# Kernel optimization log

Measured on AMD Instinct MI355X. Metric: run time of the kernel, lower is better.

The kernel has to match this reference:

```python
import jax, jax.numpy as jnp
import numpy as np
from jax import lax

# dims: B=2, C=dim=64, H=W=128 -> N=16384 tokens; d_inner=128, d_state=16, dt_rank=4, d_conv=4

def setup_inputs() -> dict:
    key = jax.random.key(0)
    ks = jax.random.split(key, 8)
    def n(k, shp, scale=0.02):
        return jax.random.normal(k, shp, jnp.float32) * scale
    d_inner, d_state, dt_rank = 128, 16, 4
    return {
        "x": jax.random.normal(ks[0], (2, 64, 128, 128), jnp.float32),
        "ln_w": jnp.ones((64,), jnp.float32),
        "ln_b": jnp.zeros((64,), jnp.float32),
        "in_proj_w": n(ks[1], (2 * d_inner, 64)),
        "conv_w": n(ks[2], (d_inner, 1, 4), 0.1),
        "conv_b": jnp.zeros((d_inner,), jnp.float32),
        "x_proj_w": n(ks[3], (dt_rank + 2 * d_state, d_inner)),
        "dt_proj_w": n(ks[4], (d_inner, dt_rank), 0.5),
        "dt_proj_b": n(ks[5], (d_inner,), 0.1),
        "A_log": jnp.log(jnp.broadcast_to(jnp.arange(1, d_state + 1, dtype=jnp.float32), (d_inner, d_state))),
        "D_param": jnp.ones((d_inner,), jnp.float32),
        "out_proj_w": n(ks[6], (64, d_inner)),
        "out_proj_b": jnp.zeros((64,), jnp.float32),
    }


def reference(x, ln_w, ln_b, in_proj_w, conv_w, conv_b, x_proj_w,
              dt_proj_w, dt_proj_b, A_log, D_param, out_proj_w, out_proj_b):
    B, C, H, W = x.shape
    d_inner = in_proj_w.shape[0] // 2
    d_state = A_log.shape[1]
    dt_rank = dt_proj_w.shape[1]
    eps = 1e-5

    # feature2token + channel LayerNorm (Restormer WithBias LN over C)
    t = x.reshape(B, C, H * W).transpose(0, 2, 1)  # [B, N, C]
    mu = jnp.mean(t, axis=-1, keepdims=True)
    var = jnp.var(t, axis=-1, keepdims=True)
    t = (t - mu) * lax.rsqrt(var + eps) * ln_w + ln_b

    # in_proj -> x, z
    xz = jnp.einsum('bnc,dc->bnd', t, in_proj_w)  # [B, N, 2*d_inner]
    x_in, z = jnp.split(xz, 2, axis=-1)

    # depthwise causal conv1d (k=4, pad left 3), then SiLU
    u = lax.conv_general_dilated(
        x_in.transpose(0, 2, 1), conv_w,
        window_strides=(1,), padding=[(3, 0)],
        feature_group_count=d_inner,
        dimension_numbers=('NCH', 'OIH', 'NCH'))
    u = jax.nn.silu(u + conv_b[None, :, None]).transpose(0, 2, 1)  # [B, N, d_inner]

    # x_proj -> dt, B, C of the SSM
    x_dbl = jnp.einsum('bnd,ed->bne', u, x_proj_w)
    dt_r = x_dbl[..., :dt_rank]
    Bmat = x_dbl[..., dt_rank:dt_rank + d_state]   # [B, N, d_state]
    Cmat = x_dbl[..., dt_rank + d_state:]          # [B, N, d_state]
    dt = jax.nn.softplus(jnp.einsum('bnr,dr->bnd', dt_r, dt_proj_w) + dt_proj_b)

    # selective scan: h_t = exp(dt*A) h_{t-1} + dt*B*u
    A = -jnp.exp(A_log)  # [d_inner, d_state]
    deltaA = jnp.exp(jnp.einsum('bnd,ds->bnds', dt, A))
    deltaBu = jnp.einsum('bnd,bns,bnd->bnds', dt, Bmat, u)

    def combine(c1, c2):
        a1, b1 = c1
        a2, b2 = c2
        return a2 * a1, a2 * b1 + b2

    _, h = lax.associative_scan(combine, (deltaA, deltaBu), axis=1)  # h: [B, N, d_inner, d_state]

    y = jnp.einsum('bnds,bns->bnd', h, Cmat) + u * D_param
    y = y * jax.nn.silu(z)
    out = jnp.einsum('bnd,cd->bnc', y, out_proj_w) + out_proj_b  # [B, N, C]

    # token2feature
    return out.transpose(0, 2, 1).reshape(B, C, H, W)
```

## Files before the change

kernel.cpp:

```cpp
#include <hip/hip_runtime.h>
#include <math.h>

#define NTOK 16384
#define DIN  128
#define NCH  512
#define CHL  32
#define NG   32
#define GCH  16

__device__ __forceinline__ float silu_f(float x)    { return x / (1.f + __expf(-x)); }
__device__ __forceinline__ float softplus_f(float x){ return (x > 20.f) ? x : log1pf(__expf(x)); }

__global__ __launch_bounds__(256) void k1_ln_inproj(
    const float* __restrict__ x, const float* __restrict__ lnw,
    const float* __restrict__ lnb, const float* __restrict__ Win,
    float* __restrict__ xin, float* __restrict__ zbuf)
{
  __shared__ __align__(16) float bufW[128*68];
  __shared__ __align__(16) float bufB[64*68];
  __shared__ float ps[256], pq[256], mu[64], rs[64];

  int t = threadIdx.x;
  int b  = blockIdx.x >> 8;
  int n0 = (blockIdx.x & 255) << 6;
  const float* xb = x + ((size_t)b*64)*NTOK;

  int tok = t & 63, quad = t >> 6;
  float s0 = 0.f, s1 = 0.f;
  for (int i = 0; i < 16; ++i) {
    int c = i*4 + quad;
    float v = xb[(size_t)c*NTOK + n0 + tok];
    bufW[c*68 + tok] = v;
    s0 += v; s1 += v*v;
  }
  ps[t] = s0; pq[t] = s1;
  __syncthreads();
  if (t < 64) {
    float m = ps[t] + ps[64+t] + ps[128+t] + ps[192+t];
    float q = pq[t] + pq[64+t] + pq[128+t] + pq[192+t];
    m *= 0.015625f;
    q = q*0.015625f - m*m;
    mu[t] = m; rs[t] = rsqrtf(q + 1e-5f);
  }
  __syncthreads();

  {
    int c = t & 63, tq = t >> 6;
    float wv = lnw[c], bv = lnb[c];
    #pragma unroll
    for (int i = 0; i < 4; ++i) {
      int tok4 = tq*4 + i;
      float4 f = *(const float4*)&bufW[c*68 + tok4*4];
      float vals[4] = {f.x, f.y, f.z, f.w};
      #pragma unroll
      for (int k = 0; k < 4; ++k) {
        int tk = tok4*4 + k;
        bufB[tk*68 + c] = (vals[k] - mu[tk]) * rs[tk] * wv + bv;
      }
    }
  }

  int tokg = t & 7, dg = t >> 3;
  const float4* TB = (const float4*)bufB;
  const float4* TW = (const float4*)bufW;
  long nbase = (long)b*NTOK + n0;
  for (int half = 0; half < 2; ++half) {
    __syncthreads();
    {
      const float4* Wg = (const float4*)&Win[(half << 7)*64];
      #pragma unroll
      for (int i = 0; i < 8; ++i) {
        int idx = i*256 + t;
        int row = idx >> 4, q = idx & 15;
        *(float4*)&bufW[row*68 + q*4] = Wg[row*16 + q];
      }
    }
    __syncthreads();
    float acc[8][4];
    #pragma unroll
    for (int i = 0; i < 8; ++i)
      #pragma unroll
      for (int j = 0; j < 4; ++j) acc[i][j] = 0.f;
    #pragma unroll 4
    for (int c4 = 0; c4 < 16; ++c4) {
      float4 tv[8], wv[4];
      #pragma unroll
      for (int i = 0; i < 8; ++i) tv[i] = TB[(tokg + 8*i)*17 + c4];
      #pragma unroll
      for (int j = 0; j < 4; ++j) wv[j] = TW[(dg + 32*j)*17 + c4];
      #pragma unroll
      for (int i = 0; i < 8; ++i)
        #pragma unroll
        for (int j = 0; j < 4; ++j)
          acc[i][j] += tv[i].x*wv[j].x + tv[i].y*wv[j].y
                     + tv[i].z*wv[j].z + tv[i].w*wv[j].w;
    }
    #pragma unroll
    for (int i = 0; i < 8; ++i) {
      long n = nbase + tokg + 8*i;
      #pragma unroll
      for (int j = 0; j < 4; ++j) {
        int d = dg + 32*j;
        if (half == 0) xin[n*128 + d] = acc[i][j];
        else           zbuf[n*128 + d] = silu_f(acc[i][j]);
      }
    }
  }
}

__global__ __launch_bounds__(256) void k2_conv(
    const float* __restrict__ xin, const float* __restrict__ cw,
    const float* __restrict__ cb, float* __restrict__ u)
{
  int t = threadIdx.x;
  int d = t & 127;
  long g0 = (long)blockIdx.x*16 + (t >> 7)*8;
  int n = (int)(g0 & (NTOK-1));
  float w0 = cw[d*4], w1 = cw[d*4+1], w2 = cw[d*4+2], w3 = cw[d*4+3];
  float cbv = cb[d];
  float xa = (n >= 3) ? xin[(g0-3)*128 + d] : 0.f;
  float xb = (n >= 2) ? xin[(g0-2)*128 + d] : 0.f;
  float xc = (n >= 1) ? xin[(g0-1)*128 + d] : 0.f;
  #pragma unroll
  for (int j = 0; j < 8; ++j) {
    float xd = xin[(g0+j)*128 + d];
    u[(g0+j)*128 + d] = silu_f(w0*xa + w1*xb + w2*xc + w3*xd + cbv);
    xa = xb; xb = xc; xc = xd;
  }
}

__global__ __launch_bounds__(256) void k3_xproj_dt(
    const float* __restrict__ u, const float* __restrict__ Wx,
    const float* __restrict__ Wdt, const float* __restrict__ db,
    float* __restrict__ dt, float* __restrict__ Bm, float* __restrict__ Cm)
{
  __shared__ float wdtT[4*128];
  __shared__ __align__(16) float xdbl[64*40];
  int t = threadIdx.x;
  for (int i = t; i < 512; i += 256)
    wdtT[(i&3)*128 + (i>>2)] = Wdt[i];

  long tok0 = (long)blockIdx.x * 64;
  int tok = t & 63;
  int grp = __builtin_amdgcn_readfirstlane(t >> 6);
  const float* urow = u + (tok0 + tok)*128;
  const float* wrow = Wx + grp*9*128;

  float acc[9];
  #pragma unroll
  for (int e = 0; e < 9; ++e) acc[e] = 0.f;
  #pragma unroll 4
  for (int d4 = 0; d4 < 32; ++d4) {
    float4 uv = *(const float4*)&urow[d4*4];
    #pragma unroll
    for (int e = 0; e < 9; ++e) {
      float4 wv = *(const float4*)&wrow[e*128 + d4*4];
      acc[e] += uv.x*wv.x + uv.y*wv.y + uv.z*wv.z + uv.w*wv.w;
    }
  }
  #pragma unroll
  for (int e = 0; e < 9; ++e) xdbl[tok*40 + grp*9 + e] = acc[e];
  __syncthreads();

  {
    int tk = t >> 2, q = t & 3;
    float4 bv = *(const float4*)&xdbl[tk*40 + 4  + q*4];
    float4 cv = *(const float4*)&xdbl[tk*40 + 20 + q*4];
    *(float4*)&Bm[(tok0+tk)*16 + q*4] = bv;
    *(float4*)&Cm[(tok0+tk)*16 + q*4] = cv;
  }
  int d = t & 127, th = t >> 7;
  float w0 = wdtT[d], w1 = wdtT[128+d], w2 = wdtT[256+d], w3 = wdtT[384+d];
  float bias = db[d];
  for (int j = 0; j < 32; ++j) {
    int tk = th*32 + j;
    float a = bias + xdbl[tk*40]*w0 + xdbl[tk*40+1]*w1
                   + xdbl[tk*40+2]*w2 + xdbl[tk*40+3]*w3;
    dt[(tok0+tk)*128 + d] = softplus_f(a);
  }
}

__global__ __launch_bounds__(256) void k4a_local(
    const float* __restrict__ dt, const float* __restrict__ u,
    const float* __restrict__ Bm, const float* __restrict__ Alog,
    float* __restrict__ carP, float* __restrict__ carH)
{
  int t = threadIdx.x;
  int d = t >> 1, sh = t & 1;
  int b = blockIdx.x / NCH, ch = blockIdx.x % NCH;
  long nb = (long)b*NTOK + (long)ch*CHL;
  float A[8], h[8], P[8];
  #pragma unroll
  for (int k = 0; k < 2; ++k) {
    float4 a = *(const float4*)&Alog[d*16 + sh*8 + k*4];
    A[k*4+0] = -__expf(a.x); A[k*4+1] = -__expf(a.y);
    A[k*4+2] = -__expf(a.z); A[k*4+3] = -__expf(a.w);
  }
  #pragma unroll
  for (int s = 0; s < 8; ++s) { h[s] = 0.f; P[s] = 1.f; }
  for (int i = 0; i < CHL; ++i) {
    long n = nb + i;
    float dtv = dt[n*128 + d];
    float uv  = u [n*128 + d];
    float du  = dtv * uv;
    float Bv[8];
    #pragma unroll
    for (int k = 0; k < 2; ++k) {
      float4 v = *(const float4*)&Bm[n*16 + sh*8 + k*4];
      Bv[k*4]=v.x; Bv[k*4+1]=v.y; Bv[k*4+2]=v.z; Bv[k*4+3]=v.w;
    }
    #pragma unroll
    for (int s = 0; s < 8; ++s) {
      float dA = __expf(dtv * A[s]);
      h[s] = dA*h[s] + du*Bv[s];
      P[s] *= dA;
    }
  }
  long cbs = ((long)(b*NCH + ch)*128 + d)*16 + sh*8;
  #pragma unroll
  for (int k = 0; k < 2; ++k) {
    *(float4*)&carP[cbs + k*4] = make_float4(P[k*4],P[k*4+1],P[k*4+2],P[k*4+3]);
    *(float4*)&carH[cbs + k*4] = make_float4(h[k*4],h[k*4+1],h[k*4+2],h[k*4+3]);
  }
}

__global__ __launch_bounds__(256) void k4b1_group(
    float* __restrict__ cP, float* __restrict__ cH,
    float* __restrict__ Pg, float* __restrict__ Hg)
{
  int idx = blockIdx.x*256 + threadIdx.x;
  int rem = idx & 2047;
  int g   = (idx >> 11) & (NG-1);
  int b   = idx >> 16;
  float P = 1.f, H = 0.f;
  long base = ((long)b*NCH + g*GCH)*2048 + rem;
  #pragma unroll 4
  for (int j = 0; j < GCH; ++j) {
    long a = base + (long)j*2048;
    float p = cP[a], h = cH[a];
    cP[a] = P; cH[a] = H;
    H = p*H + h;
    P = p*P;
  }
  long ga = ((long)b*NG + g)*2048 + rem;
  Pg[ga] = P; Hg[ga] = H;
}

__global__ __launch_bounds__(256) void k4b2_carry(
    const float* __restrict__ Pg, float* __restrict__ Hg)
{
  int idx = blockIdx.x*256 + threadIdx.x;
  int b = idx >> 11, rem = idx & 2047;
  float H = 0.f;
  #pragma unroll 4
  for (int g = 0; g < NG; ++g) {
    long a = ((long)b*NG + g)*2048 + rem;
    float p = Pg[a], h = Hg[a];
    Hg[a] = H;
    H = p*H + h;
  }
}

__global__ __launch_bounds__(256) void k4c_apply(
    const float* __restrict__ dt, const float* __restrict__ u,
    const float* __restrict__ Bm, const float* __restrict__ Cm,
    const float* __restrict__ Alog, const float* __restrict__ Dp,
    const float* __restrict__ zs, const float* __restrict__ pPre,
    const float* __restrict__ hPre, const float* __restrict__ Hg,
    float* __restrict__ yz)
{
  int t = threadIdx.x;
  int d = t >> 1, sh = t & 1;
  int b = blockIdx.x / NCH, ch = blockIdx.x % NCH;
  long nb = (long)b*NTOK + (long)ch*CHL;
  float A[8], h[8];
  #pragma unroll
  for (int k = 0; k < 2; ++k) {
    float4 a = *(const float4*)&Alog[d*16 + sh*8 + k*4];
    A[k*4+0] = -__expf(a.x); A[k*4+1] = -__expf(a.y);
    A[k*4+2] = -__expf(a.z); A[k*4+3] = -__expf(a.w);
  }
  long cbs = ((long)(b*NCH + ch)*128 + d)*16 + sh*8;
  long gbs = ((long)b*NG + (ch >> 4))*2048 + d*16 + sh*8;
  #pragma unroll
  for (int k = 0; k < 2; ++k) {
    float4 hp = *(const float4*)&hPre[cbs + k*4];
    float4 pp = *(const float4*)&pPre[cbs + k*4];
    float4 gi = *(const float4*)&Hg[gbs + k*4];
    h[k*4+0] = hp.x + pp.x*gi.x; h[k*4+1] = hp.y + pp.y*gi.y;
    h[k*4+2] = hp.z + pp.z*gi.z; h[k*4+3] = hp.w + pp.w*gi.w;
  }
  float Dv = Dp[d];
  for (int i = 0; i < CHL; ++i) {
    long n = nb + i;
    float dtv = dt[n*128 + d];
    float uv  = u [n*128 + d];
    float du  = dtv * uv;
    float Bv[8], Cv[8];
    #pragma unroll
    for (int k = 0; k < 2; ++k) {
      float4 v = *(const float4*)&Bm[n*16 + sh*8 + k*4];
      Bv[k*4]=v.x; Bv[k*4+1]=v.y; Bv[k*4+2]=v.z; Bv[k*4+3]=v.w;
      float4 w = *(const float4*)&Cm[n*16 + sh*8 + k*4];
      Cv[k*4]=w.x; Cv[k*4+1]=w.y; Cv[k*4+2]=w.z; Cv[k*4+3]=w.w;
    }
    float y = 0.f;
    #pragma unroll
    for (int s = 0; s < 8; ++s) {
      float dA = __expf(dtv * A[s]);
      h[s] = dA*h[s] + du*Bv[s];
      y += h[s]*Cv[s];
    }
    y += __shfl_xor(y, 1);
    if (sh == 0)
      yz[n*128 + d] = (y + uv*Dv) * zs[n*128 + d];
  }
}

__global__ __launch_bounds__(256) void k6_outproj(
    const float* __restrict__ yz, const float* __restrict__ Wout,
    const float* __restrict__ ob, float* __restrict__ out)
{
  __shared__ __align__(16) float wo[64*132];
  __shared__ __align__(16) float yl[32*132];
  int t = threadIdx.x;
  long tok0 = (long)blockIdx.x * 32;
  for (int i = 0; i < 8; ++i) {
    int g = i*256 + t; int c = g >> 5, q = g & 31;
    *(float4*)&wo[c*132 + q*4] = *(const float4*)&Wout[c*128 + q*4];
  }
  for (int i = 0; i < 4; ++i) {
    int g = i*256 + t; int tok = g >> 5, q = g & 31;
    *(float4*)&yl[tok*132 + q*4] = *(const float4*)&yz[(tok0 + tok)*128 + q*4];
  }
  __syncthreads();
  int tp = t & 15;
  int tg = t >> 4;
  float acc[4][2] = {{0.f}};
  for (int d4 = 0; d4 < 32; ++d4) {
    float4 y0 = *(const float4*)&yl[tg*132 + d4*4];
    float4 y1 = *(const float4*)&yl[(tg+16)*132 + d4*4];
    #pragma unroll
    for (int cc = 0; cc < 4; ++cc) {
      float4 wv = *(const float4*)&wo[(tp + 16*cc)*132 + d4*4];
      acc[cc][0] += wv.x*y0.x + wv.y*y0.y + wv.z*y0.z + wv.w*y0.w;
      acc[cc][1] += wv.x*y1.x + wv.y*y1.y + wv.z*y1.z + wv.w*y1.w;
    }
  }
  int b  = (int)(tok0 / NTOK);
  long n0 = tok0 % NTOK;
  #pragma unroll
  for (int cc = 0; cc < 4; ++cc) {
    int c = tp + 16*cc;
    float bias = ob[c];
    out[((long)b*64 + c)*NTOK + n0 + tg     ] = acc[cc][0] + bias;
    out[((long)b*64 + c)*NTOK + n0 + tg + 16] = acc[cc][1] + bias;
  }
}

extern "C" void kernel_launch(void* const* d_in, const int* in_sizes, int n_in,
                              void* d_out, int out_size, void* d_ws, size_t ws_size,
                              hipStream_t stream)
{
  (void)in_sizes; (void)n_in; (void)out_size; (void)ws_size;
  const float* x    = (const float*)d_in[0];
  const float* lnw  = (const float*)d_in[1];
  const float* lnb  = (const float*)d_in[2];
  const float* Win  = (const float*)d_in[3];
  const float* cw   = (const float*)d_in[4];
  const float* cb   = (const float*)d_in[5];
  const float* Wx   = (const float*)d_in[6];
  const float* Wdt  = (const float*)d_in[7];
  const float* db   = (const float*)d_in[8];
  const float* Alog = (const float*)d_in[9];
  const float* Dp   = (const float*)d_in[10];
  const float* Wout = (const float*)d_in[11];
  const float* ob   = (const float*)d_in[12];
  float* out = (float*)d_out;

  float* w   = (float*)d_ws;
  float* xin = w;
  float* z   = w + 4194304;
  float* u   = w + 8388608;
  float* dt  = w + 12582912;
  float* Bm  = w + 16777216;
  float* Cm  = w + 17301504;
  float* cP  = w + 17825792;
  float* cH  = w + 19922944;
  float* Pg  = w + 22020096;
  float* Hg  = w + 22151168;
  float* yz  = w + 22282240;

  k1_ln_inproj<<<512, 256, 0, stream>>>(x, lnw, lnb, Win, xin, z);
  k2_conv     <<<2048,256, 0, stream>>>(xin, cw, cb, u);
  k3_xproj_dt <<<512, 256, 0, stream>>>(u, Wx, Wdt, db, dt, Bm, Cm);
  k4a_local   <<<1024,256, 0, stream>>>(dt, u, Bm, Alog, cP, cH);
  k4b1_group  <<<512, 256, 0, stream>>>(cP, cH, Pg, Hg);
  k4b2_carry  <<<16,  256, 0, stream>>>(Pg, Hg);
  k4c_apply   <<<1024,256, 0, stream>>>(dt, u, Bm, Cm, Alog, Dp, z, cP, cH, Hg, yz);
  k6_outproj  <<<1024,256, 0, stream>>>(yz, Wout, ob, out);
}
```

Measured before the change: 149.3 us.

## Write transposed u copy in conv kernel for coalesced x_proj reads

```diff
diff --git a/kernel.cpp b/kernel.cpp
--- a/kernel.cpp
+++ b/kernel.cpp
@@ -110,27 +110,34 @@
 
 __global__ __launch_bounds__(256) void k2_conv(
     const float* __restrict__ xin, const float* __restrict__ cw,
-    const float* __restrict__ cb, float* __restrict__ u)
+    const float* __restrict__ cb, float* __restrict__ u, float* __restrict__ uT)
 {
   int t = threadIdx.x;
   int d = t & 127;
-  long g0 = (long)blockIdx.x*16 + (t >> 7)*8;
+  long g0 = (long)blockIdx.x*64 + (t >> 7)*32;
   int n = (int)(g0 & (NTOK-1));
   float w0 = cw[d*4], w1 = cw[d*4+1], w2 = cw[d*4+2], w3 = cw[d*4+3];
   float cbv = cb[d];
   float xa = (n >= 3) ? xin[(g0-3)*128 + d] : 0.f;
   float xb = (n >= 2) ? xin[(g0-2)*128 + d] : 0.f;
   float xc = (n >= 1) ? xin[(g0-1)*128 + d] : 0.f;
-  #pragma unroll
-  for (int j = 0; j < 8; ++j) {
+  float ur[32];
+  #pragma unroll
+  for (int j = 0; j < 32; ++j) {
     float xd = xin[(g0+j)*128 + d];
-    u[(g0+j)*128 + d] = silu_f(w0*xa + w1*xb + w2*xc + w3*xd + cbv);
+    float uv = silu_f(w0*xa + w1*xb + w2*xc + w3*xd + cbv);
+    u[(g0+j)*128 + d] = uv;
+    ur[j] = uv;
     xa = xb; xb = xc; xc = xd;
   }
+  float* urow = uT + (long)d*32768 + g0;
+  #pragma unroll
+  for (int q = 0; q < 8; ++q)
+    *(float4*)&urow[q*4] = make_float4(ur[q*4], ur[q*4+1], ur[q*4+2], ur[q*4+3]);
 }
 
 __global__ __launch_bounds__(256) void k3_xproj_dt(
-    const float* __restrict__ u, const float* __restrict__ Wx,
+    const float* __restrict__ uT, const float* __restrict__ Wx,
     const float* __restrict__ Wdt, const float* __restrict__ db,
     float* __restrict__ dt, float* __restrict__ Bm, float* __restrict__ Cm)
 {
@@ -143,20 +150,18 @@
   long tok0 = (long)blockIdx.x * 64;
   int tok = t & 63;
   int grp = __builtin_amdgcn_readfirstlane(t >> 6);
-  const float* urow = u + (tok0 + tok)*128;
   const float* wrow = Wx + grp*9*128;
+  const float* ucol = uT + tok0 + tok;
 
   float acc[9];
   #pragma unroll
   for (int e = 0; e < 9; ++e) acc[e] = 0.f;
-  #pragma unroll 4
-  for (int d4 = 0; d4 < 32; ++d4) {
-    float4 uv = *(const float4*)&urow[d4*4];
-    #pragma unroll
-    for (int e = 0; e < 9; ++e) {
-      float4 wv = *(const float4*)&wrow[e*128 + d4*4];
-      acc[e] += uv.x*wv.x + uv.y*wv.y + uv.z*wv.z + uv.w*wv.w;
-    }
+  #pragma unroll 8
+  for (int d = 0; d < 128; ++d) {
+    float uv = ucol[(long)d*32768];
+    #pragma unroll
+    for (int e = 0; e < 9; ++e)
+      acc[e] = fmaf(uv, wrow[e*128 + d], acc[e]);
   }
   #pragma unroll
   for (int e = 0; e < 9; ++e) xdbl[tok*40 + grp*9 + e] = acc[e];
@@ -390,10 +395,11 @@
   float* Pg  = w + 22020096;
   float* Hg  = w + 22151168;
   float* yz  = w + 22282240;
+  float* uT  = w + 26476544;
 
   k1_ln_inproj<<<512, 256, 0, stream>>>(x, lnw, lnb, Win, xin, z);
-  k2_conv     <<<2048,256, 0, stream>>>(xin, cw, cb, u);
-  k3_xproj_dt <<<512, 256, 0, stream>>>(u, Wx, Wdt, db, dt, Bm, Cm);
+  k2_conv     <<<512, 256, 0, stream>>>(xin, cw, cb, u, uT);
+  k3_xproj_dt <<<512, 256, 0, stream>>>(uT, Wx, Wdt, db, dt, Bm, Cm);
   k4a_local   <<<1024,256, 0, stream>>>(dt, u, Bm, Alog, cP, cH);
   k4b1_group  <<<512, 256, 0, stream>>>(cP, cH, Pg, Hg);
   k4b2_carry  <<<16,  256, 0, stream>>>(Pg, Hg);
```

New measurement: 152.4 us. 2.1% more time.
